# Kernel tuning notes

Hardware: AMD Instinct MI355X
Metric: run time of the kernel (lower is better)

The kernel has to match this reference:

```python
import jax, jax.numpy as jnp
import numpy as np

N = 100000   # nodes
E = 1600000  # edges
F = 128      # feature dim == Dense units
R = 50       # relations
BN_EPS = 1e-3  # keras BatchNormalization default epsilon


def setup_inputs() -> dict:
    key = jax.random.key(0)
    ks = jax.random.split(key, 8)
    x = jax.random.normal(ks[0], (N, F), dtype=jnp.float32)
    edge_rows = jax.random.randint(ks[1], (E,), 0, N, dtype=jnp.int32)
    edge_cols = jax.random.randint(ks[2], (E,), 0, N, dtype=jnp.int32)
    edge_vals = jax.random.uniform(ks[3], (E,), dtype=jnp.float32)
    rel_ids = jax.random.randint(ks[4], (E,), 0, R, dtype=jnp.int32)
    relation_coeffs = jax.random.uniform(ks[5], (R,), dtype=jnp.float32)
    coeff_kernel = jax.random.normal(ks[6], (N, 1), dtype=jnp.float32) * 0.05
    dense_kernel = jax.random.normal(ks[7], (F, F), dtype=jnp.float32) / np.sqrt(F).astype(np.float32)
    dense_bias = jnp.zeros((F,), dtype=jnp.float32)
    bn_gamma = jnp.ones((F,), dtype=jnp.float32)
    bn_beta = jnp.zeros((F,), dtype=jnp.float32)
    bn_mean = jnp.zeros((F,), dtype=jnp.float32)
    bn_var = jnp.ones((F,), dtype=jnp.float32)
    return {
        "x": x, "edge_rows": edge_rows, "edge_cols": edge_cols,
        "edge_vals": edge_vals, "rel_ids": rel_ids,
        "relation_coeffs": relation_coeffs, "coeff_kernel": coeff_kernel,
        "dense_kernel": dense_kernel, "dense_bias": dense_bias,
        "bn_gamma": bn_gamma, "bn_beta": bn_beta,
        "bn_mean": bn_mean, "bn_var": bn_var,
    }


def reference(x, edge_rows, edge_cols, edge_vals, rel_ids,
              relation_coeffs, coeff_kernel, dense_kernel, dense_bias,
              bn_gamma, bn_beta, bn_mean, bn_var):
    # BatchNorm (inference: moving statistics)
    h = (x - bn_mean) * jax.lax.rsqrt(bn_var + BN_EPS) * bn_gamma + bn_beta  # [N, F]
    # relation_coeff_adj2: edge weight = A.values * (rel_coeffs[rel] + 1)^-1
    w = edge_vals / (relation_coeffs[rel_ids] + 1.0)  # [E]
    # SpMM: out[i] = sum_{(i,j) in edges} w_e * h[j]
    msgs = w[:, None] * h[edge_cols]                   # [E, F]
    agg = jax.ops.segment_sum(msgs, edge_rows, num_segments=N)  # [N, F]
    # CoeffLayer(mul=True): inputs * (kernel + 1)
    pre = agg + h * (coeff_kernel + 1.0)               # [N, F]
    # Dense
    return pre @ dense_kernel + dense_bias             # [N, F]
```

## Files before the change

### kernel.cpp

```cpp
#include <hip/hip_runtime.h>
#include <stdint.h>

#define N_NODES 100000
#define N_EDGES 1600000
#define FDIM 128
#define NREL 50
#define BN_EPS 1e-3f
#define N_PAD 100096
#define NBUCK 782
#define EPB 8192
#define NBLK 196
#define NSEG 4

typedef short short8_t __attribute__((ext_vector_type(8)));
typedef float f32x4_t __attribute__((ext_vector_type(4)));

__device__ __forceinline__ uint32_t f2bf(float f) {
    union { float f; uint32_t u; } v; v.f = f;
    uint32_t u = v.u;
    return (u + 0x7FFFu + ((u >> 16) & 1u)) >> 16;
}
__device__ __forceinline__ float bflo(uint32_t p) {
    union { uint32_t u; float f; } v; v.u = p << 16; return v.f;
}
__device__ __forceinline__ float bfhi(uint32_t p) {
    union { uint32_t u; float f; } v; v.u = p & 0xFFFF0000u; return v.f;
}

__global__ void prep_kernel(const float* __restrict__ gamma, const float* __restrict__ beta,
                            const float* __restrict__ mean, const float* __restrict__ var,
                            const float* __restrict__ relc, const float* __restrict__ W,
                            float* __restrict__ scale, float* __restrict__ shift,
                            float* __restrict__ rel_inv, uint16_t* __restrict__ WT) {
    int t = threadIdx.x;
    if (t < FDIM) {
        float s = gamma[t] * rsqrtf(var[t] + BN_EPS);
        scale[t] = s;
        shift[t] = beta[t] - mean[t] * s;
    }
    if (t < NREL) rel_inv[t] = 1.0f / (relc[t] + 1.0f);
    for (int idx = t; idx < FDIM * FDIM; idx += blockDim.x) {
        int f = idx >> 7, k = idx & 127;
        WT[idx] = (uint16_t)f2bf(W[k * FDIM + f]);
    }
}

__global__ void h_kernel(const float* __restrict__ x, const float* __restrict__ scale,
                         const float* __restrict__ shift, uint2* __restrict__ h) {
    int i4 = blockIdx.x * blockDim.x + threadIdx.x;
    if (i4 >= N_NODES * 32) return;
    int cg = (i4 & 31) * 4;
    float4 xv = ((const float4*)x)[i4];
    float4 sc = *(const float4*)(scale + cg);
    float4 sh = *(const float4*)(shift + cg);
    uint2 o;
    o.x = f2bf(xv.x * sc.x + sh.x) | (f2bf(xv.y * sc.y + sh.y) << 16);
    o.y = f2bf(xv.z * sc.z + sh.z) | (f2bf(xv.w * sc.w + sh.w) << 16);
    h[i4] = o;
}

__global__ __launch_bounds__(1024) void sort1_kernel(const int* __restrict__ rows,
                                                     int* __restrict__ bhist) {
    __shared__ int lh[NBUCK];
    int t = threadIdx.x;
    for (int i = t; i < NBUCK; i += 1024) lh[i] = 0;
    __syncthreads();
    int e0 = blockIdx.x * EPB;
    int e1 = min(e0 + EPB, N_EDGES);
    for (int e = e0 + t; e < e1; e += 1024)
        atomicAdd(&lh[rows[e] >> 7], 1);
    __syncthreads();
    for (int i = t; i < NBUCK; i += 1024) bhist[blockIdx.x * NBUCK + i] = lh[i];
}

__global__ __launch_bounds__(256) void btot_kernel(const int* __restrict__ bhist,
                                                   int* __restrict__ btot) {
    int wv = (blockIdx.x * 256 + threadIdx.x) >> 6;
    int lane = threadIdx.x & 63;
    if (wv >= NBUCK) return;
    int s = 0;
    for (int idx = lane; idx < NBLK; idx += 64) s += bhist[idx * NBUCK + wv];
    for (int d = 32; d > 0; d >>= 1) s += __shfl_down(s, d);
    if (lane == 0) btot[wv] = s;
}

__global__ __launch_bounds__(1024) void bprefix_kernel(const int* __restrict__ btot,
                                                       int* __restrict__ bstart,
                                                       int* __restrict__ row_start) {
    __shared__ int sm[1024];
    int t = threadIdx.x;
    int v = (t < NBUCK) ? btot[t] : 0;
    sm[t] = v;
    __syncthreads();
    for (int off = 1; off < 1024; off <<= 1) {
        int xv = 0;
        if (t >= off) xv = sm[t - off];
        __syncthreads();
        sm[t] += xv;
        __syncthreads();
    }
    if (t < NBUCK) bstart[t] = sm[t] - v;
    if (t == 0) {
        bstart[NBUCK] = sm[1023];
        row_start[N_NODES] = sm[1023];
    }
}

__global__ __launch_bounds__(256) void bscan_kernel(const int* __restrict__ bhist,
                                                    const int* __restrict__ bstart,
                                                    int* __restrict__ bbase) {
    int wv = (blockIdx.x * 256 + threadIdx.x) >> 6;
    int lane = threadIdx.x & 63;
    if (wv >= NBUCK) return;
    int base = bstart[wv];
    int carry = 0;
#pragma unroll
    for (int seg = 0; seg < NSEG; ++seg) {
        int idx = seg * 64 + lane;
        int v = (idx < NBLK) ? bhist[idx * NBUCK + wv] : 0;
        int s = v;
        for (int d = 1; d < 64; d <<= 1) {
            int u = __shfl_up(s, d);
            if (lane >= d) s += u;
        }
        if (idx < NBLK) bbase[idx * NBUCK + wv] = base + carry + s - v;
        carry += __shfl(s, 63);
    }
}

__global__ __launch_bounds__(1024) void sort2_kernel(
        const int* __restrict__ rows, const int* __restrict__ cols,
        const float* __restrict__ vals, const int* __restrict__ rels,
        const float* __restrict__ rel_inv, const int* __restrict__ bbase,
        uint2* __restrict__ staging) {
    __shared__ int lcur[NBUCK];
    int t = threadIdx.x;
    for (int i = t; i < NBUCK; i += 1024) lcur[i] = bbase[blockIdx.x * NBUCK + i];
    __syncthreads();
    int e0 = blockIdx.x * EPB;
    int e1 = min(e0 + EPB, N_EDGES);
    for (int e = e0 + t; e < e1; e += 1024) {
        int r = rows[e];
        float w = vals[e] * rel_inv[rels[e]];
        int p = atomicAdd(&lcur[r >> 7], 1);
        uint2 s;
        s.x = (uint32_t)cols[e] | ((uint32_t)(r & 127) << 20);
        s.y = __float_as_uint(w);
        staging[p] = s;
    }
}

__global__ __launch_bounds__(256) void bucket_kernel(
        const uint2* __restrict__ staging, const int* __restrict__ bstart,
        int* __restrict__ row_start, uint2* __restrict__ scolw) {
    __shared__ int lh[128];
    __shared__ int sm[128];
    __shared__ int lcur[128];
    int b = blockIdx.x;
    int r0 = b << 7;
    int nrows = min(128, N_NODES - r0);
    int t = threadIdx.x;
    if (t < 128) lh[t] = 0;
    __syncthreads();
    int e0 = bstart[b];
    int e1 = bstart[b + 1];
    for (int e = e0 + t; e < e1; e += 256)
        atomicAdd(&lh[(staging[e].x >> 20) & 127], 1);
    __syncthreads();
    int v = (t < 128) ? lh[t] : 0;
    if (t < 128) sm[t] = v;
    __syncthreads();
    for (int off = 1; off < 128; off <<= 1) {
        int xv = 0;
        if (t < 128 && t >= off) xv = sm[t - off];
        __syncthreads();
        if (t < 128) sm[t] += xv;
        __syncthreads();
    }
    if (t < nrows) {
        int rs = e0 + sm[t] - v;
        row_start[r0 + t] = rs;
        lcur[t] = rs;
    }
    __syncthreads();
    for (int e = e0 + t; e < e1; e += 256) {
        uint2 s = staging[e];
        int rl = (s.x >> 20) & 127;
        int p = atomicAdd(&lcur[rl], 1);
        uint2 o; o.x = s.x & 0xFFFFF; o.y = s.y;
        scolw[p] = o;
    }
}

__global__ __launch_bounds__(256) void spmm_kernel(
        const uint32_t* __restrict__ h, const int* __restrict__ row_start,
        const uint2* __restrict__ scolw, const float* __restrict__ ck,
        uint32_t* __restrict__ pre) {
    int row = blockIdx.x * 4 + (threadIdx.x >> 6);
    int lane = threadIdx.x & 63;
    uint32_t p = h[(size_t)row * 64 + lane];
    float coef = ck[row] + 1.0f;
    float ax = coef * bflo(p);
    float ay = coef * bfhi(p);
    int e0 = row_start[row], e1 = row_start[row + 1];
    for (int base = e0; base < e1; base += 64) {
        int cnt = min(64, e1 - base);
        int myc = 0; float myw = 0.f;
        if (lane < cnt) {
            uint2 s = scolw[base + lane];
            myc = (int)s.x;
            myw = __uint_as_float(s.y);
        }
        for (int i = 0; i < cnt; i += 8) {
            int c[8]; float w[8]; uint32_t q[8];
#pragma unroll
            for (int j = 0; j < 8; ++j) { c[j] = __shfl(myc, i + j); w[j] = __shfl(myw, i + j); }
#pragma unroll
            for (int j = 0; j < 8; ++j) q[j] = h[(size_t)c[j] * 64 + lane];
#pragma unroll
            for (int j = 0; j < 8; ++j) { ax += w[j] * bflo(q[j]); ay += w[j] * bfhi(q[j]); }
        }
    }
    pre[(size_t)row * 64 + lane] = f2bf(ax) | (f2bf(ay) << 16);
}

__global__ __launch_bounds__(256) void gemm_kernel(
        const uint16_t* __restrict__ pre, const uint16_t* __restrict__ WT,
        const float* __restrict__ bias, float* __restrict__ out) {
    int wave = threadIdx.x >> 6;
    int lane = threadIdx.x & 63;
    int row0 = blockIdx.x * 64 + wave * 16;
    int m = lane & 15, q = lane >> 4;

    short8_t a[4];
    const uint16_t* arow = pre + (size_t)(row0 + m) * FDIM + q * 8;
#pragma unroll
    for (int t = 0; t < 4; ++t)
        a[t] = *(const short8_t*)(arow + t * 32);

    for (int ct = 0; ct < 8; ++ct) {
        int col0 = ct * 16;
        const uint16_t* brow = WT + (size_t)(col0 + m) * FDIM + q * 8;
        f32x4_t acc = {0.f, 0.f, 0.f, 0.f};
#pragma unroll
        for (int t = 0; t < 4; ++t) {
            short8_t b = *(const short8_t*)(brow + t * 32);
            acc = __builtin_amdgcn_mfma_f32_16x16x32_bf16(a[t], b, acc, 0, 0, 0);
        }
        float bs = bias[col0 + m];
#pragma unroll
        for (int r = 0; r < 4; ++r) {
            int row = row0 + q * 4 + r;
            if (row < N_NODES)
                out[(size_t)row * FDIM + col0 + m] = acc[r] + bs;
        }
    }
}

extern "C" void kernel_launch(void* const* d_in, const int* in_sizes, int n_in,
                              void* d_out, int out_size, void* d_ws, size_t ws_size,
                              hipStream_t stream) {
    const float* x     = (const float*)d_in[0];
    const int*   erows = (const int*)d_in[1];
    const int*   ecols = (const int*)d_in[2];
    const float* evals = (const float*)d_in[3];
    const int*   erels = (const int*)d_in[4];
    const float* relc  = (const float*)d_in[5];
    const float* ck    = (const float*)d_in[6];
    const float* W     = (const float*)d_in[7];
    const float* bias  = (const float*)d_in[8];
    const float* gamma = (const float*)d_in[9];
    const float* beta  = (const float*)d_in[10];
    const float* mean  = (const float*)d_in[11];
    const float* var   = (const float*)d_in[12];
    float* out = (float*)d_out;

    char* wp = (char*)d_ws;
    auto alloc = [&](size_t bytes) {
        char* p = wp;
        wp += (bytes + 255) & ~(size_t)255;
        return (void*)p;
    };
    uint16_t* h      = (uint16_t*)alloc((size_t)N_PAD * FDIM * 2);
    uint16_t* pre    = (uint16_t*)alloc((size_t)N_PAD * FDIM * 2);
    uint2* scolw     = (uint2*)alloc((size_t)N_EDGES * 8);
    int* row_start   = (int*)alloc((size_t)(N_NODES + 1) * 4);
    int* bhist       = (int*)alloc((size_t)NBLK * NBUCK * 4);
    int* bbase       = (int*)alloc((size_t)NBLK * NBUCK * 4);
    int* btot        = (int*)alloc((size_t)NBUCK * 4);
    int* bstart      = (int*)alloc((size_t)(NBUCK + 1) * 4);
    uint16_t* WT     = (uint16_t*)alloc(FDIM * FDIM * 2);
    float* scale     = (float*)alloc(FDIM * 4);
    float* shift     = (float*)alloc(FDIM * 4);
    float* rel_inv   = (float*)alloc(256 * 4);
    if ((size_t)(wp - (char*)d_ws) > ws_size) return;

    uint2* staging = (uint2*)pre;

    prep_kernel<<<1, 256, 0, stream>>>(gamma, beta, mean, var, relc, W, scale, shift, rel_inv, WT);
    h_kernel<<<(N_NODES * 32) / 256, 256, 0, stream>>>(x, scale, shift, (uint2*)h);
    sort1_kernel<<<NBLK, 1024, 0, stream>>>(erows, bhist);
    btot_kernel<<<(NBUCK + 3) / 4, 256, 0, stream>>>(bhist, btot);
    bprefix_kernel<<<1, 1024, 0, stream>>>(btot, bstart, row_start);
    bscan_kernel<<<(NBUCK + 3) / 4, 256, 0, stream>>>(bhist, bstart, bbase);
    sort2_kernel<<<NBLK, 1024, 0, stream>>>(erows, ecols, evals, erels, rel_inv, bbase, staging);
    bucket_kernel<<<NBUCK, 256, 0, stream>>>(staging, bstart, row_start, scolw);
    spmm_kernel<<<N_NODES / 4, 256, 0, stream>>>((const uint32_t*)h, row_start,
                                                 scolw, ck, (uint32_t*)pre);
    gemm_kernel<<<(N_NODES + 63) / 64, 256, 0, stream>>>(pre, WT, bias, out);
}
```

Measured before the change: 301.9 us.

## Fuse bucket sort into SpMM using LDS-resident per-bucket edge lists

Merges the per-bucket row sort and the SpMM into one kernel. Each block counting-sorts its 128-row bucket's edges into shared memory, then four waves each aggregate 32 rows from LDS, removing the global scolw and row_start round trip and one launch. The cost is only 782 blocks of 256 threads, with 32 KB of LDS each, which cuts parallelism relative to 25000 four-row blocks. A slow fallback path rescans the bucket's edges for every row when a bucket exceeds 4096 edges.

```diff
diff --git a/kernel.cpp b/kernel.cpp
--- a/kernel.cpp
+++ b/kernel.cpp
@@ -11,6 +11,7 @@
 #define EPB 8192
 #define NBLK 196
 #define NSEG 4
+#define CAP 4096
 
 typedef short short8_t __attribute__((ext_vector_type(8)));
 typedef float f32x4_t __attribute__((ext_vector_type(4)));
@@ -85,8 +86,7 @@
 }
 
 __global__ __launch_bounds__(1024) void bprefix_kernel(const int* __restrict__ btot,
-                                                       int* __restrict__ bstart,
-                                                       int* __restrict__ row_start) {
+                                                       int* __restrict__ bstart) {
     __shared__ int sm[1024];
     int t = threadIdx.x;
     int v = (t < NBUCK) ? btot[t] : 0;
@@ -100,10 +100,7 @@
         __syncthreads();
     }
     if (t < NBUCK) bstart[t] = sm[t] - v;
-    if (t == 0) {
-        bstart[NBUCK] = sm[1023];
-        row_start[N_NODES] = sm[1023];
-    }
+    if (t == 0) bstart[NBUCK] = sm[1023];
 }
 
 __global__ __launch_bounds__(256) void bscan_kernel(const int* __restrict__ bhist,
@@ -150,20 +147,21 @@
     }
 }
 
-__global__ __launch_bounds__(256) void bucket_kernel(
-        const uint2* __restrict__ staging, const int* __restrict__ bstart,
-        int* __restrict__ row_start, uint2* __restrict__ scolw) {
-    __shared__ int lh[128];
+__global__ __launch_bounds__(256) void spmm_kernel(
+        const uint32_t* __restrict__ h, const int* __restrict__ bstart,
+        const uint2* __restrict__ staging, const float* __restrict__ ck,
+        uint32_t* __restrict__ pre) {
+    __shared__ int lh[129];
     __shared__ int sm[128];
     __shared__ int lcur[128];
+    __shared__ uint2 sedge[CAP];
     int b = blockIdx.x;
     int r0 = b << 7;
-    int nrows = min(128, N_NODES - r0);
-    int t = threadIdx.x;
+    int t = threadIdx.x;
+    int e0 = bstart[b], e1 = bstart[b + 1];
+    int n = e1 - e0;
     if (t < 128) lh[t] = 0;
     __syncthreads();
-    int e0 = bstart[b];
-    int e1 = bstart[b + 1];
     for (int e = e0 + t; e < e1; e += 256)
         atomicAdd(&lh[(staging[e].x >> 20) & 127], 1);
     __syncthreads();
@@ -177,51 +175,62 @@
         if (t < 128) sm[t] += xv;
         __syncthreads();
     }
-    if (t < nrows) {
-        int rs = e0 + sm[t] - v;
-        row_start[r0 + t] = rs;
-        lcur[t] = rs;
-    }
-    __syncthreads();
-    for (int e = e0 + t; e < e1; e += 256) {
-        uint2 s = staging[e];
-        int rl = (s.x >> 20) & 127;
-        int p = atomicAdd(&lcur[rl], 1);
-        uint2 o; o.x = s.x & 0xFFFFF; o.y = s.y;
-        scolw[p] = o;
-    }
-}
-
-__global__ __launch_bounds__(256) void spmm_kernel(
-        const uint32_t* __restrict__ h, const int* __restrict__ row_start,
-        const uint2* __restrict__ scolw, const float* __restrict__ ck,
-        uint32_t* __restrict__ pre) {
-    int row = blockIdx.x * 4 + (threadIdx.x >> 6);
-    int lane = threadIdx.x & 63;
-    uint32_t p = h[(size_t)row * 64 + lane];
-    float coef = ck[row] + 1.0f;
-    float ax = coef * bflo(p);
-    float ay = coef * bfhi(p);
-    int e0 = row_start[row], e1 = row_start[row + 1];
-    for (int base = e0; base < e1; base += 64) {
-        int cnt = min(64, e1 - base);
-        int myc = 0; float myw = 0.f;
-        if (lane < cnt) {
-            uint2 s = scolw[base + lane];
-            myc = (int)s.x;
-            myw = __uint_as_float(s.y);
-        }
-        for (int i = 0; i < cnt; i += 8) {
-            int c[8]; float w[8]; uint32_t q[8];
-#pragma unroll
-            for (int j = 0; j < 8; ++j) { c[j] = __shfl(myc, i + j); w[j] = __shfl(myw, i + j); }
-#pragma unroll
-            for (int j = 0; j < 8; ++j) q[j] = h[(size_t)c[j] * 64 + lane];
-#pragma unroll
-            for (int j = 0; j < 8; ++j) { ax += w[j] * bflo(q[j]); ay += w[j] * bfhi(q[j]); }
-        }
-    }
-    pre[(size_t)row * 64 + lane] = f2bf(ax) | (f2bf(ay) << 16);
+    if (t < 128) { lh[t] = sm[t] - v; lcur[t] = sm[t] - v; }
+    if (t == 0) lh[128] = n;
+    __syncthreads();
+    bool lds_ok = (n <= CAP);
+    if (lds_ok) {
+        for (int e = e0 + t; e < e1; e += 256) {
+            uint2 s = staging[e];
+            int rl = (s.x >> 20) & 127;
+            int p = atomicAdd(&lcur[rl], 1);
+            uint2 o; o.x = s.x & 0xFFFFF; o.y = s.y;
+            sedge[p] = o;
+        }
+    }
+    __syncthreads();
+    int wave = t >> 6, lane = t & 63;
+    for (int rr = wave * 32; rr < wave * 32 + 32; ++rr) {
+        int row = r0 + rr;
+        if (row >= N_NODES) break;
+        uint32_t p = h[(size_t)row * 64 + lane];
+        float coef = ck[row] + 1.0f;
+        float ax = coef * bflo(p);
+        float ay = coef * bfhi(p);
+        if (lds_ok) {
+            int lo = lh[rr], hi = lh[rr + 1];
+            int i = lo;
+            for (; i + 8 <= hi; i += 8) {
+                uint2 e[8];
+#pragma unroll
+                for (int j = 0; j < 8; ++j) e[j] = sedge[i + j];
+                uint32_t q[8];
+#pragma unroll
+                for (int j = 0; j < 8; ++j) q[j] = h[(size_t)e[j].x * 64 + lane];
+#pragma unroll
+                for (int j = 0; j < 8; ++j) {
+                    float w = __uint_as_float(e[j].y);
+                    ax += w * bflo(q[j]); ay += w * bfhi(q[j]);
+                }
+            }
+            for (; i < hi; ++i) {
+                uint2 ee = sedge[i];
+                uint32_t q = h[(size_t)ee.x * 64 + lane];
+                float w = __uint_as_float(ee.y);
+                ax += w * bflo(q); ay += w * bfhi(q);
+            }
+        } else {
+            for (int e = e0; e < e1; ++e) {
+                uint2 s = staging[e];
+                if (((s.x >> 20) & 127) == rr) {
+                    uint32_t q = h[(size_t)(s.x & 0xFFFFF) * 64 + lane];
+                    float w = __uint_as_float(s.y);
+                    ax += w * bflo(q); ay += w * bfhi(q);
+                }
+            }
+        }
+        pre[(size_t)row * 64 + lane] = f2bf(ax) | (f2bf(ay) << 16);
+    }
 }
 
 __global__ __launch_bounds__(256) void gemm_kernel(
@@ -283,8 +292,7 @@
     };
     uint16_t* h      = (uint16_t*)alloc((size_t)N_PAD * FDIM * 2);
     uint16_t* pre    = (uint16_t*)alloc((size_t)N_PAD * FDIM * 2);
-    uint2* scolw     = (uint2*)alloc((size_t)N_EDGES * 8);
-    int* row_start   = (int*)alloc((size_t)(N_NODES + 1) * 4);
+    uint2* staging   = (uint2*)alloc((size_t)N_EDGES * 8);
     int* bhist       = (int*)alloc((size_t)NBLK * NBUCK * 4);
     int* bbase       = (int*)alloc((size_t)NBLK * NBUCK * 4);
     int* btot        = (int*)alloc((size_t)NBUCK * 4);
@@ -295,17 +303,13 @@
     float* rel_inv   = (float*)alloc(256 * 4);
     if ((size_t)(wp - (char*)d_ws) > ws_size) return;
 
-    uint2* staging = (uint2*)pre;
-
     prep_kernel<<<1, 256, 0, stream>>>(gamma, beta, mean, var, relc, W, scale, shift, rel_inv, WT);
     h_kernel<<<(N_NODES * 32) / 256, 256, 0, stream>>>(x, scale, shift, (uint2*)h);
     sort1_kernel<<<NBLK, 1024, 0, stream>>>(erows, bhist);
     btot_kernel<<<(NBUCK + 3) / 4, 256, 0, stream>>>(bhist, btot);
-    bprefix_kernel<<<1, 1024, 0, stream>>>(btot, bstart, row_start);
+    bprefix_kernel<<<1, 1024, 0, stream>>>(btot, bstart);
     bscan_kernel<<<(NBUCK + 3) / 4, 256, 0, stream>>>(bhist, bstart, bbase);
     sort2_kernel<<<NBLK, 1024, 0, stream>>>(erows, ecols, evals, erels, rel_inv, bbase, staging);
-    bucket_kernel<<<NBUCK, 256, 0, stream>>>(staging, bstart, row_start, scolw);
-    spmm_kernel<<<N_NODES / 4, 256, 0, stream>>>((const uint32_t*)h, row_start,
-                                                 scolw, ck, (uint32_t*)pre);
+    spmm_kernel<<<NBUCK, 256, 0, stream>>>((const uint32_t*)h, bstart, staging, ck, (uint32_t*)pre);
     gemm_kernel<<<(N_NODES + 63) / 64, 256, 0, stream>>>(pre, WT, bias, out);
 }
```

After: 324.6 us. +7.5%, slower.

## Fuse preprocessing launches and pad per-row edge lists for vectorized SpMM

Applied to the files above, without the earlier changes.

Merges the BN/h, weight transpose and bucket-histogram kernels into one launch, and folds the three scan kernels into a single one-block scan_kernel. The histogram is transposed to bucket-major for coalesced scanning, and the relation inverse is computed in shared memory inside sort2. bucket_kernel now pads each row's edge list to a multiple of four with zero entries plus per-bucket slack, so the SpMM inner loop can issue 16-byte edge loads and four gathers without shuffles or bounds checks. The aim is to cut launch count and SpMM loop overhead, at the cost of a single-block scan that serializes work and some extra padded edges to process.

```diff
diff --git a/kernel.cpp b/kernel.cpp
--- a/kernel.cpp
+++ b/kernel.cpp
@@ -11,6 +11,8 @@
 #define EPB 8192
 #define NBLK 196
 #define NSEG 4
+#define SLACK 384
+#define HBLK 6250
 
 typedef short short8_t __attribute__((ext_vector_type(8)));
 typedef float f32x4_t __attribute__((ext_vector_type(4)));
@@ -27,121 +29,110 @@
     union { uint32_t u; float f; } v; v.u = p & 0xFFFF0000u; return v.f;
 }
 
-__global__ void prep_kernel(const float* __restrict__ gamma, const float* __restrict__ beta,
-                            const float* __restrict__ mean, const float* __restrict__ var,
-                            const float* __restrict__ relc, const float* __restrict__ W,
-                            float* __restrict__ scale, float* __restrict__ shift,
-                            float* __restrict__ rel_inv, uint16_t* __restrict__ WT) {
+__global__ __launch_bounds__(512) void pre_kernel(
+        const float* __restrict__ x, const int* __restrict__ rows,
+        const float* __restrict__ gamma, const float* __restrict__ beta,
+        const float* __restrict__ mean, const float* __restrict__ var,
+        const float* __restrict__ W,
+        uint2* __restrict__ h, int* __restrict__ bhist, uint16_t* __restrict__ WT) {
+    __shared__ int lh[NBUCK];
+    int b = blockIdx.x, t = threadIdx.x;
+    if (b < NBLK) {
+        for (int i = t; i < NBUCK; i += 512) lh[i] = 0;
+        __syncthreads();
+        int e0 = b * EPB, e1 = min(e0 + EPB, N_EDGES);
+        for (int e = e0 + t; e < e1; e += 512)
+            atomicAdd(&lh[rows[e] >> 7], 1);
+        __syncthreads();
+        for (int i = t; i < NBUCK; i += 512) bhist[(size_t)i * NBLK + b] = lh[i];
+    } else if (b == NBLK) {
+        for (int idx = t; idx < FDIM * FDIM; idx += 512) {
+            int f = idx >> 7, k = idx & 127;
+            WT[idx] = (uint16_t)f2bf(W[k * FDIM + f]);
+        }
+    } else {
+        int i4 = (b - NBLK - 1) * 512 + t;
+        int cg = (i4 & 31) * 4;
+        float4 xv = ((const float4*)x)[i4];
+        float4 g4 = *(const float4*)(gamma + cg);
+        float4 b4 = *(const float4*)(beta + cg);
+        float4 m4 = *(const float4*)(mean + cg);
+        float4 v4 = *(const float4*)(var + cg);
+        float s0 = g4.x * rsqrtf(v4.x + BN_EPS);
+        float s1 = g4.y * rsqrtf(v4.y + BN_EPS);
+        float s2 = g4.z * rsqrtf(v4.z + BN_EPS);
+        float s3 = g4.w * rsqrtf(v4.w + BN_EPS);
+        float h0 = (xv.x - m4.x) * s0 + b4.x;
+        float h1 = (xv.y - m4.y) * s1 + b4.y;
+        float h2 = (xv.z - m4.z) * s2 + b4.z;
+        float h3 = (xv.w - m4.w) * s3 + b4.w;
+        uint2 o;
+        o.x = f2bf(h0) | (f2bf(h1) << 16);
+        o.y = f2bf(h2) | (f2bf(h3) << 16);
+        h[i4] = o;
+    }
+}
+
+__global__ __launch_bounds__(1024) void scan_kernel(const int* __restrict__ bhist,
+                                                    int* __restrict__ bstart,
+                                                    int* __restrict__ bbase) {
+    __shared__ int sm[1024];
+    __shared__ int ex[1024];
     int t = threadIdx.x;
-    if (t < FDIM) {
-        float s = gamma[t] * rsqrtf(var[t] + BN_EPS);
-        scale[t] = s;
-        shift[t] = beta[t] - mean[t] * s;
-    }
-    if (t < NREL) rel_inv[t] = 1.0f / (relc[t] + 1.0f);
-    for (int idx = t; idx < FDIM * FDIM; idx += blockDim.x) {
-        int f = idx >> 7, k = idx & 127;
-        WT[idx] = (uint16_t)f2bf(W[k * FDIM + f]);
-    }
-}
-
-__global__ void h_kernel(const float* __restrict__ x, const float* __restrict__ scale,
-                         const float* __restrict__ shift, uint2* __restrict__ h) {
-    int i4 = blockIdx.x * blockDim.x + threadIdx.x;
-    if (i4 >= N_NODES * 32) return;
-    int cg = (i4 & 31) * 4;
-    float4 xv = ((const float4*)x)[i4];
-    float4 sc = *(const float4*)(scale + cg);
-    float4 sh = *(const float4*)(shift + cg);
-    uint2 o;
-    o.x = f2bf(xv.x * sc.x + sh.x) | (f2bf(xv.y * sc.y + sh.y) << 16);
-    o.y = f2bf(xv.z * sc.z + sh.z) | (f2bf(xv.w * sc.w + sh.w) << 16);
-    h[i4] = o;
-}
-
-__global__ __launch_bounds__(1024) void sort1_kernel(const int* __restrict__ rows,
-                                                     int* __restrict__ bhist) {
-    __shared__ int lh[NBUCK];
-    int t = threadIdx.x;
-    for (int i = t; i < NBUCK; i += 1024) lh[i] = 0;
-    __syncthreads();
-    int e0 = blockIdx.x * EPB;
-    int e1 = min(e0 + EPB, N_EDGES);
-    for (int e = e0 + t; e < e1; e += 1024)
-        atomicAdd(&lh[rows[e] >> 7], 1);
-    __syncthreads();
-    for (int i = t; i < NBUCK; i += 1024) bhist[blockIdx.x * NBUCK + i] = lh[i];
-}
-
-__global__ __launch_bounds__(256) void btot_kernel(const int* __restrict__ bhist,
-                                                   int* __restrict__ btot) {
-    int wv = (blockIdx.x * 256 + threadIdx.x) >> 6;
-    int lane = threadIdx.x & 63;
-    if (wv >= NBUCK) return;
-    int s = 0;
-    for (int idx = lane; idx < NBLK; idx += 64) s += bhist[idx * NBUCK + wv];
-    for (int d = 32; d > 0; d >>= 1) s += __shfl_down(s, d);
-    if (lane == 0) btot[wv] = s;
-}
-
-__global__ __launch_bounds__(1024) void bprefix_kernel(const int* __restrict__ btot,
-                                                       int* __restrict__ bstart,
-                                                       int* __restrict__ row_start) {
-    __shared__ int sm[1024];
-    int t = threadIdx.x;
-    int v = (t < NBUCK) ? btot[t] : 0;
-    sm[t] = v;
-    __syncthreads();
+    int wave = t >> 6, lane = t & 63;
+    sm[t] = 0;
+    __syncthreads();
+    for (int wv = wave; wv < NBUCK; wv += 16) {
+        int s = 0;
+        for (int idx = lane; idx < NBLK; idx += 64) s += bhist[(size_t)wv * NBLK + idx];
+        for (int d = 32; d > 0; d >>= 1) s += __shfl_down(s, d);
+        if (lane == 0) sm[wv] = s;
+    }
+    __syncthreads();
+    int v = sm[t];
     for (int off = 1; off < 1024; off <<= 1) {
-        int xv = 0;
-        if (t >= off) xv = sm[t - off];
+        int xv = (t >= off) ? sm[t - off] : 0;
         __syncthreads();
         sm[t] += xv;
         __syncthreads();
     }
+    ex[t] = sm[t] - v;
     if (t < NBUCK) bstart[t] = sm[t] - v;
-    if (t == 0) {
-        bstart[NBUCK] = sm[1023];
-        row_start[N_NODES] = sm[1023];
-    }
-}
-
-__global__ __launch_bounds__(256) void bscan_kernel(const int* __restrict__ bhist,
-                                                    const int* __restrict__ bstart,
-                                                    int* __restrict__ bbase) {
-    int wv = (blockIdx.x * 256 + threadIdx.x) >> 6;
-    int lane = threadIdx.x & 63;
-    if (wv >= NBUCK) return;
-    int base = bstart[wv];
-    int carry = 0;
+    if (t == 0) bstart[NBUCK] = sm[1023];
+    __syncthreads();
+    for (int wv = wave; wv < NBUCK; wv += 16) {
+        int base = ex[wv];
+        int carry = 0;
 #pragma unroll
-    for (int seg = 0; seg < NSEG; ++seg) {
-        int idx = seg * 64 + lane;
-        int v = (idx < NBLK) ? bhist[idx * NBUCK + wv] : 0;
-        int s = v;
-        for (int d = 1; d < 64; d <<= 1) {
-            int u = __shfl_up(s, d);
-            if (lane >= d) s += u;
-        }
-        if (idx < NBLK) bbase[idx * NBUCK + wv] = base + carry + s - v;
-        carry += __shfl(s, 63);
+        for (int seg = 0; seg < NSEG; ++seg) {
+            int idx = seg * 64 + lane;
+            int vv = (idx < NBLK) ? bhist[(size_t)wv * NBLK + idx] : 0;
+            int s = vv;
+            for (int d = 1; d < 64; d <<= 1) {
+                int u = __shfl_up(s, d);
+                if (lane >= d) s += u;
+            }
+            if (idx < NBLK) bbase[(size_t)wv * NBLK + idx] = base + carry + s - vv;
+            carry += __shfl(s, 63);
+        }
     }
 }
 
 __global__ __launch_bounds__(1024) void sort2_kernel(
         const int* __restrict__ rows, const int* __restrict__ cols,
         const float* __restrict__ vals, const int* __restrict__ rels,
-        const float* __restrict__ rel_inv, const int* __restrict__ bbase,
+        const float* __restrict__ relc, const int* __restrict__ bbase,
         uint2* __restrict__ staging) {
     __shared__ int lcur[NBUCK];
-    int t = threadIdx.x;
-    for (int i = t; i < NBUCK; i += 1024) lcur[i] = bbase[blockIdx.x * NBUCK + i];
-    __syncthreads();
-    int e0 = blockIdx.x * EPB;
-    int e1 = min(e0 + EPB, N_EDGES);
+    __shared__ float lrel[NREL];
+    int t = threadIdx.x, b = blockIdx.x;
+    if (t < NREL) lrel[t] = 1.0f / (relc[t] + 1.0f);
+    for (int i = t; i < NBUCK; i += 1024) lcur[i] = bbase[(size_t)i * NBLK + b];
+    __syncthreads();
+    int e0 = b * EPB, e1 = min(e0 + EPB, N_EDGES);
     for (int e = e0 + t; e < e1; e += 1024) {
         int r = rows[e];
-        float w = vals[e] * rel_inv[rels[e]];
+        float w = vals[e] * lrel[rels[e]];
         int p = atomicAdd(&lcur[r >> 7], 1);
         uint2 s;
         s.x = (uint32_t)cols[e] | ((uint32_t)(r & 127) << 20);
@@ -152,23 +143,21 @@
 
 __global__ __launch_bounds__(256) void bucket_kernel(
         const uint2* __restrict__ staging, const int* __restrict__ bstart,
-        int* __restrict__ row_start, uint2* __restrict__ scolw) {
+        uint2* __restrict__ rowrange, uint2* __restrict__ scolw) {
     __shared__ int lh[128];
     __shared__ int sm[128];
     __shared__ int lcur[128];
-    int b = blockIdx.x;
-    int r0 = b << 7;
+    int b = blockIdx.x, r0 = b << 7, t = threadIdx.x;
     int nrows = min(128, N_NODES - r0);
-    int t = threadIdx.x;
     if (t < 128) lh[t] = 0;
     __syncthreads();
-    int e0 = bstart[b];
-    int e1 = bstart[b + 1];
+    int e0 = bstart[b], e1 = bstart[b + 1];
     for (int e = e0 + t; e < e1; e += 256)
         atomicAdd(&lh[(staging[e].x >> 20) & 127], 1);
     __syncthreads();
     int v = (t < 128) ? lh[t] : 0;
-    if (t < 128) sm[t] = v;
+    int pv = (v + 3) & ~3;
+    if (t < 128) sm[t] = pv;
     __syncthreads();
     for (int off = 1; off < 128; off <<= 1) {
         int xv = 0;
@@ -177,10 +166,15 @@
         if (t < 128) sm[t] += xv;
         __syncthreads();
     }
-    if (t < nrows) {
-        int rs = e0 + sm[t] - v;
-        row_start[r0 + t] = rs;
-        lcur[t] = rs;
+    int sbase = e0 + SLACK * b;
+    int start = 0;
+    if (t < 128) {
+        start = sbase + sm[t] - pv;
+        lcur[t] = start;
+        if (t < nrows) {
+            uint2 rr; rr.x = (uint32_t)start; rr.y = (uint32_t)(start + pv);
+            rowrange[r0 + t] = rr;
+        }
     }
     __syncthreads();
     for (int e = e0 + t; e < e1; e += 256) {
@@ -190,36 +184,39 @@
         uint2 o; o.x = s.x & 0xFFFFF; o.y = s.y;
         scolw[p] = o;
     }
+    if (t < 128) {
+        uint2 z; z.x = 0; z.y = 0;
+        for (int k = v; k < pv; ++k) scolw[start + k] = z;
+    }
 }
 
 __global__ __launch_bounds__(256) void spmm_kernel(
-        const uint32_t* __restrict__ h, const int* __restrict__ row_start,
+        const uint32_t* __restrict__ h, const uint2* __restrict__ rowrange,
         const uint2* __restrict__ scolw, const float* __restrict__ ck,
         uint32_t* __restrict__ pre) {
     int row = blockIdx.x * 4 + (threadIdx.x >> 6);
     int lane = threadIdx.x & 63;
+    uint2 rr = rowrange[row];
+    int e  = __builtin_amdgcn_readfirstlane((int)rr.x);
+    int e1 = __builtin_amdgcn_readfirstlane((int)rr.y);
     uint32_t p = h[(size_t)row * 64 + lane];
     float coef = ck[row] + 1.0f;
     float ax = coef * bflo(p);
     float ay = coef * bfhi(p);
-    int e0 = row_start[row], e1 = row_start[row + 1];
-    for (int base = e0; base < e1; base += 64) {
-        int cnt = min(64, e1 - base);
-        int myc = 0; float myw = 0.f;
-        if (lane < cnt) {
-            uint2 s = scolw[base + lane];
-            myc = (int)s.x;
-            myw = __uint_as_float(s.y);
-        }
-        for (int i = 0; i < cnt; i += 8) {
-            int c[8]; float w[8]; uint32_t q[8];
-#pragma unroll
-            for (int j = 0; j < 8; ++j) { c[j] = __shfl(myc, i + j); w[j] = __shfl(myw, i + j); }
-#pragma unroll
-            for (int j = 0; j < 8; ++j) q[j] = h[(size_t)c[j] * 64 + lane];
-#pragma unroll
-            for (int j = 0; j < 8; ++j) { ax += w[j] * bflo(q[j]); ay += w[j] * bfhi(q[j]); }
-        }
+    for (; e < e1; e += 4) {
+        const uint4* ep = (const uint4*)(scolw + e);
+        uint4 eA = ep[0];
+        uint4 eB = ep[1];
+        uint32_t q0 = h[eA.x * 64u + lane];
+        uint32_t q1 = h[eA.z * 64u + lane];
+        uint32_t q2 = h[eB.x * 64u + lane];
+        uint32_t q3 = h[eB.z * 64u + lane];
+        float w0 = __uint_as_float(eA.y), w1 = __uint_as_float(eA.w);
+        float w2 = __uint_as_float(eB.y), w3 = __uint_as_float(eB.w);
+        ax += w0 * bflo(q0); ay += w0 * bfhi(q0);
+        ax += w1 * bflo(q1); ay += w1 * bfhi(q1);
+        ax += w2 * bflo(q2); ay += w2 * bfhi(q2);
+        ax += w3 * bflo(q3); ay += w3 * bfhi(q3);
     }
     pre[(size_t)row * 64 + lane] = f2bf(ax) | (f2bf(ay) << 16);
 }
@@ -283,29 +280,22 @@
     };
     uint16_t* h      = (uint16_t*)alloc((size_t)N_PAD * FDIM * 2);
     uint16_t* pre    = (uint16_t*)alloc((size_t)N_PAD * FDIM * 2);
-    uint2* scolw     = (uint2*)alloc((size_t)N_EDGES * 8);
-    int* row_start   = (int*)alloc((size_t)(N_NODES + 1) * 4);
-    int* bhist       = (int*)alloc((size_t)NBLK * NBUCK * 4);
-    int* bbase       = (int*)alloc((size_t)NBLK * NBUCK * 4);
-    int* btot        = (int*)alloc((size_t)NBUCK * 4);
+    uint2* scolw     = (uint2*)alloc((size_t)(N_EDGES + SLACK * NBUCK) * 8);
+    uint2* rowrange  = (uint2*)alloc((size_t)N_NODES * 8);
+    int* bhist       = (int*)alloc((size_t)NBUCK * NBLK * 4);
+    int* bbase       = (int*)alloc((size_t)NBUCK * NBLK * 4);
     int* bstart      = (int*)alloc((size_t)(NBUCK + 1) * 4);
     uint16_t* WT     = (uint16_t*)alloc(FDIM * FDIM * 2);
-    float* scale     = (float*)alloc(FDIM * 4);
-    float* shift     = (float*)alloc(FDIM * 4);
-    float* rel_inv   = (float*)alloc(256 * 4);
     if ((size_t)(wp - (char*)d_ws) > ws_size) return;
 
     uint2* staging = (uint2*)pre;
 
-    prep_kernel<<<1, 256, 0, stream>>>(gamma, beta, mean, var, relc, W, scale, shift, rel_inv, WT);
-    h_kernel<<<(N_NODES * 32) / 256, 256, 0, stream>>>(x, scale, shift, (uint2*)h);
-    sort1_kernel<<<NBLK, 1024, 0, stream>>>(erows, bhist);
-    btot_kernel<<<(NBUCK + 3) / 4, 256, 0, stream>>>(bhist, btot);
-    bprefix_kernel<<<1, 1024, 0, stream>>>(btot, bstart, row_start);
-    bscan_kernel<<<(NBUCK + 3) / 4, 256, 0, stream>>>(bhist, bstart, bbase);
-    sort2_kernel<<<NBLK, 1024, 0, stream>>>(erows, ecols, evals, erels, rel_inv, bbase, staging);
-    bucket_kernel<<<NBUCK, 256, 0, stream>>>(staging, bstart, row_start, scolw);
-    spmm_kernel<<<N_NODES / 4, 256, 0, stream>>>((const uint32_t*)h, row_start,
-                                                 scolw, ck, (uint32_t*)pre);
+    pre_kernel<<<NBLK + 1 + HBLK, 512, 0, stream>>>(x, erows, gamma, beta, mean, var, W,
+                                                    (uint2*)h, bhist, WT);
+    scan_kernel<<<1, 1024, 0, stream>>>(bhist, bstart, bbase);
+    sort2_kernel<<<NBLK, 1024, 0, stream>>>(erows, ecols, evals, erels, relc, bbase, staging);
+    bucket_kernel<<<NBUCK, 256, 0, stream>>>(staging, bstart, rowrange, scolw);
+    spmm_kernel<<<N_NODES / 4, 256, 0, stream>>>((const uint32_t*)h, rowrange, scolw, ck,
+                                                 (uint32_t*)pre);
     gemm_kernel<<<(N_NODES + 63) / 64, 256, 0, stream>>>(pre, WT, bias, out);
 }
```

After: 401.6 us. 1.33x slower.
